# Kernel tuning notes

Hardware: AMD Instinct MI355X
Metric: run time of the kernel (lower is better)

The kernel has to match this reference:

```python
import jax, jax.numpy as jnp
import numpy as np


def mha_col0(x0, w_in, b_in, w_out, b_out):
    # x0: [N, D]. torch MHA (1 head, batch_first=False): seq dim = N, this is the
    # batch-0 slice (the only one consumed by tmp[:, 0]).
    qkv = x0 @ w_in.T + b_in                     # [N, 3D]
    q, k, v = jnp.split(qkv, 3, axis=-1)         # each [N, D]
    scale = 1.0 / np.sqrt(np.float32(q.shape[-1]))
    attn = jax.nn.softmax((q * scale) @ k.T, axis=-1)   # [N, N]
    return (attn @ v) @ w_out.T + b_out          # [N, D]


def sage(x_src, x_dst, ei, w_l, b_l, w_r):
    # PyG SAGEConv with aggr='sum': out = lin_l(sum_j x_src[src_j]) + lin_r(x_dst)
    msg = x_src[ei[0]]                                            # [E, D] gather
    agg = jax.ops.segment_sum(msg, ei[1], num_segments=x_dst.shape[0])  # [Nd, D] scatter
    return agg @ w_l.T + b_l + x_dst @ w_r.T


def setup_inputs() -> dict:
    key = jax.random.key(0)
    ks = jax.random.split(key, 24)
    N, C, D, E = 8192, 6, 128, 262144
    s = 0.05
    p = lambda k, shape: jax.random.normal(k, shape, dtype=jnp.float32) * s
    return {
        "x_A": jax.random.normal(ks[0], (N, C, D), dtype=jnp.float32),
        "x_B": jax.random.normal(ks[1], (N, C, D), dtype=jnp.float32),
        "ei_AB": jax.random.randint(ks[2], (2, E), 0, N),
        "ei_BA": jax.random.randint(ks[3], (2, E), 0, N),
        "ei_AA": jax.random.randint(ks[4], (2, E), 0, N),
        "inW_A": p(ks[5], (3 * D, D)), "inB_A": p(ks[6], (3 * D,)),
        "outW_A": p(ks[7], (D, D)), "outB_A": p(ks[8], (D,)),
        "inW_B": p(ks[9], (3 * D, D)), "inB_B": p(ks[10], (3 * D,)),
        "outW_B": p(ks[11], (D, D)), "outB_B": p(ks[12], (D,)),
        "wl_AB": p(ks[13], (D, D)), "bl_AB": p(ks[14], (D,)), "wr_AB": p(ks[15], (D, D)),
        "wl_BA": p(ks[16], (D, D)), "bl_BA": p(ks[17], (D,)), "wr_BA": p(ks[18], (D, D)),
        "wl_AA": p(ks[19], (D, D)), "bl_AA": p(ks[20], (D,)), "wr_AA": p(ks[21], (D, D)),
    }


def reference(x_A, x_B, ei_AB, ei_BA, ei_AA,
              inW_A, inB_A, outW_A, outB_A,
              inW_B, inB_B, outW_B, outB_B,
              wl_AB, bl_AB, wr_AB,
              wl_BA, bl_BA, wr_BA,
              wl_AA, bl_AA, wr_AA):
    # per-type attention, keeping only column 0 (tmp[:, 0])
    h_A = mha_col0(x_A[:, 0], inW_A, inB_A, outW_A, outB_A)   # [N, D]
    h_B = mha_col0(x_B[:, 0], inW_B, inB_B, outW_B, outB_B)   # [N, D]
    # HeteroConv(aggr='sum'): B gets A->B; A gets B->A + A->A
    out_B = sage(h_A, h_B, ei_AB, wl_AB, bl_AB, wr_AB)
    out_A = (sage(h_B, h_A, ei_BA, wl_BA, bl_BA, wr_BA)
             + sage(h_A, h_A, ei_AA, wl_AA, bl_AA, wr_AA))
    # re-attach remaining column tokens (x is 3D)
    new_A = jnp.concatenate((out_A[:, None, :], x_A[:, 1:]), axis=1)  # [N, C, D]
    new_B = jnp.concatenate((out_B[:, None, :], x_B[:, 1:]), axis=1)
    return new_A, new_B
```

## Files before the change

### kernel.cpp

```cpp
#include <hip/hip_runtime.h>
#include <hip/hip_bf16.h>

typedef unsigned short u16;
typedef unsigned int u32;
typedef __attribute__((ext_vector_type(8))) short bf16x8;
typedef __attribute__((ext_vector_type(4))) short bf16x4;
typedef __attribute__((ext_vector_type(4))) float f32x4;
typedef __attribute__((ext_vector_type(16))) float f32x16;

#define MFMA(a,b,c)   __builtin_amdgcn_mfma_f32_16x16x32_bf16((a),(b),(c),0,0,0)
#define MFMA32(a,b,c) __builtin_amdgcn_mfma_f32_32x32x16_bf16((a),(b),(c),0,0,0)

__device__ __forceinline__ float bf2f(u16 u){
  union { float f; u32 i; } c; c.i = ((u32)u) << 16; return c.f;
}
__device__ __forceinline__ u16 f2bf(float f){
  __hip_bfloat16 h = __float2bfloat16(f);
  u16 u; __builtin_memcpy(&u, &h, 2); return u;
}
__device__ __forceinline__ bf16x8 ld8f(const float* p){
  bf16x8 r;
  #pragma unroll
  for (int i = 0; i < 8; i++) r[i] = (short)f2bf(p[i]);
  return r;
}
__device__ __forceinline__ u32 cvtpk(float a, float b){
  u32 r; asm volatile("v_cvt_pk_bf16_f32 %0, %1, %2" : "=v"(r) : "v"(a), "v"(b)); return r;
}
__device__ __forceinline__ void pl32swap(u32 &a, u32 &b){
  asm volatile("v_permlane32_swap_b32 %0, %1" : "+v"(a), "+v"(b));
}

struct WPrepArgs { const float* src[10]; int off[10]; int total4; };
__global__ __launch_bounds__(256) void wprep_kernel(WPrepArgs a, u16* __restrict__ dst)
{
  int i = blockIdx.x * 256 + threadIdx.x;
  if (i >= a.total4) return;
  int e = i * 4;
  int j = 0;
  #pragma unroll
  for (int k = 1; k < 10; k++) if (e >= a.off[k]) j = k;
  const float* s = a.src[j] + (e - a.off[j]);
  f32x4 v = *(const f32x4*)s;
  bf16x4 o;
  #pragma unroll
  for (int r = 0; r < 4; r++) o[r] = (short)f2bf(v[r]);
  *(bf16x4*)(dst + e) = o;
}

template<int XBF>
__global__ __launch_bounds__(256) void linear_kernel(
    const void* __restrict__ xA_, const u16* __restrict__ wA, const float* __restrict__ bA, u16* __restrict__ yA,
    const void* __restrict__ xB_, const u16* __restrict__ wB, const float* __restrict__ bB, u16* __restrict__ yB,
    u16* __restrict__ vtA_, u16* __restrict__ vtB_,
    int xstride, int ystride, int M, int N)
{
  const void* x_ = blockIdx.y ? xB_ : xA_;
  const u16* w = blockIdx.y ? wB : wA;
  const float* b = blockIdx.y ? bB : bA;
  u16* y = blockIdx.y ? yB : yA;
  u16* vt = blockIdx.y ? vtB_ : vtA_;
  const int lane = threadIdx.x & 63, wid = threadIdx.x >> 6;
  const int g = lane >> 4, l15 = lane & 15;
  const int row0 = blockIdx.x * 64 + wid * 16;

  bf16x8 a[4];
  if (XBF) {
    const u16* xr = (const u16*)x_ + (size_t)(row0 + l15) * xstride;
    #pragma unroll
    for (int kk = 0; kk < 4; kk++) a[kk] = *(const bf16x8*)(xr + kk * 32 + g * 8);
  } else {
    const float* xr = (const float*)x_ + (size_t)(row0 + l15) * xstride;
    #pragma unroll
    for (int kk = 0; kk < 4; kk++) a[kk] = ld8f(xr + kk * 32 + g * 8);
  }

  const f32x4 fz = {0.f, 0.f, 0.f, 0.f};
  for (int j0 = 0; j0 < M; j0 += 16) {
    f32x4 acc = fz;
    const u16* wr_ = w + (size_t)(j0 + l15) * 128;
    #pragma unroll
    for (int kk = 0; kk < 4; kk++)
      acc = MFMA(a[kk], *(const bf16x8*)(wr_ + kk * 32 + g * 8), acc);
    float bv = b[j0 + l15];
    if (j0 < 256 || vt == nullptr) {
      #pragma unroll
      for (int r = 0; r < 4; r++)
        y[(size_t)(row0 + g * 4 + r) * ystride + j0 + l15] = f2bf(acc[r] + bv);
    } else {
      bf16x4 o4;
      #pragma unroll
      for (int r = 0; r < 4; r++) o4[r] = (short)f2bf(acc[r] + bv);
      *(bf16x4*)(vt + (size_t)(j0 - 256 + l15) * N + row0 + g * 4) = o4;
    }
  }
}

__global__ __launch_bounds__(256, 2) void flash_kernel(
    const u16* __restrict__ qkvA, const u16* __restrict__ vtA,
    const u16* __restrict__ qkvB, const u16* __restrict__ vtB,
    u16* __restrict__ part_acc, float* __restrict__ part_ml,
    int N, int segsz, int SEG)
{
  __shared__ __align__(16) u16 Kt[2][64 * 128];
  __shared__ __align__(16) u16 Vtt[2][128 * 64];
  const int ty = blockIdx.z;
  const u16* qkv = ty ? qkvB : qkvA;
  const u16* vt  = ty ? vtB  : vtA;
  const int tid = threadIdx.x;
  const int lane = tid & 63, wid = tid >> 6;
  const int l31 = lane & 31, h = lane >> 5, l7 = lane & 7;
  const int q = blockIdx.x * 128 + wid * 32 + l31;
  const int seg = blockIdx.y;
  const int kvbase = seg * segsz;
  const float C = 0.088388347648318447f * 1.4426950408889634f;
  const float THR = 8.0f / C;

  int rk[4], ck[4], cks[4], rv[4], cv[4], cvs[4];
  #pragma unroll
  for (int i = 0; i < 4; i++) {
    int ch = tid + i * 256;
    rk[i] = ch >> 4; ck[i] = (ch & 15) * 8; cks[i] = ck[i] ^ ((rk[i] & 7) << 3);
    rv[i] = ch >> 3; cv[i] = (ch & 7) * 8;  cvs[i] = cv[i] ^ ((rv[i] & 7) << 3);
  }

  bf16x8 aQ[8];
  const u16* qr = qkv + (size_t)q * 256;
  #pragma unroll
  for (int kk = 0; kk < 8; kk++) aQ[kk] = *(const bf16x8*)(qr + kk * 16 + h * 8);

  f32x16 accO[4];
  #pragma unroll
  for (int d = 0; d < 4; d++) accO[d] = (f32x16)0.f;
  float m_ = -INFINITY, l_ = 0.f;

  {
    #pragma unroll
    for (int i = 0; i < 4; i++) {
      bf16x8 kv8 = *(const bf16x8*)(qkv + 128 + (size_t)(kvbase + rk[i]) * 256 + ck[i]);
      bf16x8 vv8 = *(const bf16x8*)(vt + (size_t)rv[i] * N + kvbase + cv[i]);
      *(bf16x8*)&Kt[0][rk[i] * 128 + cks[i]] = kv8;
      *(bf16x8*)&Vtt[0][rv[i] * 64 + cvs[i]] = vv8;
    }
  }
  __syncthreads();

  int cur = 0;
  for (int kt = 0; kt < segsz; kt += 64) {
    const bool pfch = (kt + 64 < segsz);
    bf16x8 kreg[4], vreg[4];
    if (pfch) {
      const int kv0n = kvbase + kt + 64;
      #pragma unroll
      for (int i = 0; i < 4; i++) {
        kreg[i] = *(const bf16x8*)(qkv + 128 + (size_t)(kv0n + rk[i]) * 256 + ck[i]);
        vreg[i] = *(const bf16x8*)(vt + (size_t)rv[i] * N + kv0n + cv[i]);
      }
    }

    const u16* KtC = Kt[cur];
    const u16* VtC = Vtt[cur];

    f32x16 sc0 = (f32x16)0.f, sc1 = (f32x16)0.f;
    #pragma unroll
    for (int kk = 0; kk < 8; kk++) {
      const int co = ((kk * 2 + h) * 8) ^ (l7 << 3);
      bf16x8 aK0 = *(bf16x8*)&KtC[l31 * 128 + co];
      bf16x8 aK1 = *(bf16x8*)&KtC[(32 + l31) * 128 + co];
      sc0 = MFMA32(aK0, aQ[kk], sc0);
      sc1 = MFMA32(aK1, aQ[kk], sc1);
    }

    float pmax = sc0[0];
    #pragma unroll
    for (int i = 1; i < 16; i++) pmax = fmaxf(pmax, sc0[i]);
    #pragma unroll
    for (int i = 0; i < 16; i++) pmax = fmaxf(pmax, sc1[i]);
    pmax = fmaxf(pmax, __shfl_xor(pmax, 32));
    if (!__all(pmax - m_ <= THR)) {
      float nm = fmaxf(m_, pmax);
      float corr = __builtin_exp2f((m_ - nm) * C);
      m_ = nm; l_ *= corr;
      #pragma unroll
      for (int d = 0; d < 4; d++)
        #pragma unroll
        for (int i = 0; i < 16; i++) accO[d][i] *= corr;
    }
    float sum = 0.f;
    #pragma unroll
    for (int i = 0; i < 16; i++) {
      float e0 = __builtin_exp2f((sc0[i] - m_) * C);
      float e1 = __builtin_exp2f((sc1[i] - m_) * C);
      sc0[i] = e0; sc1[i] = e1; sum += e0 + e1;
    }
    sum += __shfl_xor(sum, 32);
    l_ += sum;

    #pragma unroll
    for (int t = 0; t < 4; t++) {
      const int jA = (t & 1) * 2, jB = jA + 1;
      u32 a0, b0, a1, b1;
      if (t < 2) {
        a0 = cvtpk(sc0[jA * 4 + 0], sc0[jA * 4 + 1]);
        b0 = cvtpk(sc0[jB * 4 + 0], sc0[jB * 4 + 1]);
        a1 = cvtpk(sc0[jA * 4 + 2], sc0[jA * 4 + 3]);
        b1 = cvtpk(sc0[jB * 4 + 2], sc0[jB * 4 + 3]);
      } else {
        a0 = cvtpk(sc1[jA * 4 + 0], sc1[jA * 4 + 1]);
        b0 = cvtpk(sc1[jB * 4 + 0], sc1[jB * 4 + 1]);
        a1 = cvtpk(sc1[jA * 4 + 2], sc1[jA * 4 + 3]);
        b1 = cvtpk(sc1[jB * 4 + 2], sc1[jB * 4 + 3]);
      }
      pl32swap(a0, b0); pl32swap(a1, b1);
      union { u32 w[4]; bf16x8 v; } pf;
      pf.w[0] = a0; pf.w[1] = a1; pf.w[2] = b0; pf.w[3] = b1;
      #pragma unroll
      for (int db = 0; db < 4; db++) {
        bf16x8 aV = *(bf16x8*)&VtC[(db * 32 + l31) * 64 + (((t * 2 + h) * 8) ^ (l7 << 3))];
        accO[db] = MFMA32(aV, pf.v, accO[db]);
      }
    }

    if (pfch) {
      const int nb = cur ^ 1;
      #pragma unroll
      for (int i = 0; i < 4; i++) {
        *(bf16x8*)&Kt[nb][rk[i] * 128 + cks[i]] = kreg[i];
        *(bf16x8*)&Vtt[nb][rv[i] * 64 + cvs[i]] = vreg[i];
      }
    }
    __syncthreads();
    cur ^= 1;
  }

  const size_t pbase = ((size_t)(ty * SEG + seg) * N + q) * 128;
  #pragma unroll
  for (int d = 0; d < 4; d++)
    #pragma unroll
    for (int j = 0; j < 4; j++) {
      bf16x4 o4;
      #pragma unroll
      for (int r = 0; r < 4; r++) o4[r] = (short)f2bf(accO[d][j * 4 + r]);
      *(bf16x4*)(part_acc + pbase + d * 32 + j * 8 + h * 4) = o4;
    }
  if (h == 0) {
    float2 ml; ml.x = m_; ml.y = l_;
    *(float2*)(part_ml + ((size_t)(ty * SEG + seg) * N + q) * 2) = ml;
  }
}

__global__ __launch_bounds__(256) void combine_hproj_kernel(
    const u16* __restrict__ part_acc, const float* __restrict__ part_ml,
    const u16* __restrict__ woutA, const float* __restrict__ boutA, u16* __restrict__ hA,
    const u16* __restrict__ woutB, const float* __restrict__ boutB, u16* __restrict__ hB,
    int N, int SEG)
{
  __shared__ __align__(16) u16 ot[64 * 136];
  const int t = blockIdx.y;
  const u16* w = t ? woutB : woutA;
  const float* bb = t ? boutB : boutA;
  u16* hOut = t ? hB : hA;
  const int tid = threadIdx.x;
  const int row = tid >> 2, qt = tid & 3;
  const int grow = blockIdx.x * 64 + row;
  const float C = 0.088388347648318447f * 1.4426950408889634f;

  float m = -INFINITY;
  for (int s = 0; s < SEG; s++)
    m = fmaxf(m, part_ml[((size_t)(t * SEG + s) * N + grow) * 2]);
  float l = 0.f;
  float acc[32];
  #pragma unroll
  for (int i = 0; i < 32; i++) acc[i] = 0.f;
  for (int s = 0; s < SEG; s++) {
    const float* ml = part_ml + ((size_t)(t * SEG + s) * N + grow) * 2;
    float w8 = __builtin_exp2f((ml[0] - m) * C);
    l += w8 * ml[1];
    const u16* pa = part_acc + ((size_t)(t * SEG + s) * N + grow) * 128 + qt * 32;
    #pragma unroll
    for (int j = 0; j < 4; j++) {
      bf16x8 vch = *(const bf16x8*)(pa + j * 8);
      #pragma unroll
      for (int i = 0; i < 8; i++) acc[j * 8 + i] += w8 * bf2f((u16)vch[i]);
    }
  }
  const float inv = 1.f / l;
  #pragma unroll
  for (int j = 0; j < 4; j++) {
    bf16x8 oc;
    #pragma unroll
    for (int i = 0; i < 8; i++) oc[i] = (short)f2bf(acc[j * 8 + i] * inv);
    *(bf16x8*)&ot[row * 136 + qt * 32 + j * 8] = oc;
  }
  __syncthreads();

  const int lane = tid & 63, wid = tid >> 6;
  const int g = lane >> 4, l15 = lane & 15;
  const int row0 = wid * 16;
  bf16x8 a[4];
  #pragma unroll
  for (int kk = 0; kk < 4; kk++) a[kk] = *(bf16x8*)&ot[(row0 + l15) * 136 + kk * 32 + g * 8];
  const f32x4 fz = {0.f, 0.f, 0.f, 0.f};
  for (int j0 = 0; j0 < 128; j0 += 16) {
    f32x4 acc2 = fz;
    const u16* wr_ = w + (size_t)(j0 + l15) * 128;
    #pragma unroll
    for (int kk = 0; kk < 4; kk++)
      acc2 = MFMA(a[kk], *(const bf16x8*)(wr_ + kk * 32 + g * 8), acc2);
    float bv = bb[j0 + l15];
    #pragma unroll
    for (int r = 0; r < 4; r++)
      hOut[(size_t)(blockIdx.x * 64 + row0 + g * 4 + r) * 128 + j0 + l15] = f2bf(acc2[r] + bv);
  }
}

__global__ __launch_bounds__(256) void hist_kernel(
    const int* __restrict__ e0, const int* __restrict__ e1, const int* __restrict__ e2,
    int* __restrict__ cnt, int Nn, int E)
{
  const int t = blockIdx.y;
  const int* ei = t == 0 ? e0 : (t == 1 ? e1 : e2);
  int e = blockIdx.x * 256 + threadIdx.x;
  if (e >= E) return;
  atomicAdd(&cnt[t * Nn + ei[E + e]], 1);
}

__global__ __launch_bounds__(1024) void scan_kernel(
    const int* __restrict__ cnt, int* __restrict__ off, int* __restrict__ work, int Nn)
{
  const int t = blockIdx.x;
  const int* c = cnt + t * Nn;
  int* o = off + t * (Nn + 1);
  int* w = work + t * Nn;
  __shared__ int part[1024];
  const int tid = threadIdx.x;
  const int base = tid * 8;
  int loc[8], s = 0;
  #pragma unroll
  for (int i = 0; i < 8; i++) { loc[i] = s; s += c[base + i]; }
  part[tid] = s;
  __syncthreads();
  #pragma unroll
  for (int st = 1; st < 1024; st <<= 1) {
    int v = (tid >= st) ? part[tid - st] : 0;
    __syncthreads();
    part[tid] += v;
    __syncthreads();
  }
  int pre = (tid == 0) ? 0 : part[tid - 1];
  #pragma unroll
  for (int i = 0; i < 8; i++) { int p = pre + loc[i]; o[base + i] = p; w[base + i] = p; }
  if (tid == 1023) o[Nn] = part[1023];
}

__global__ __launch_bounds__(256) void sortedges_kernel(
    const int* __restrict__ e0, const int* __restrict__ e1, const int* __restrict__ e2,
    int* __restrict__ work, int* __restrict__ ssrc, int Nn, int E)
{
  const int t = blockIdx.y;
  const int* ei = t == 0 ? e0 : (t == 1 ? e1 : e2);
  int e = blockIdx.x * 256 + threadIdx.x;
  if (e >= E) return;
  int s = ei[e], d = ei[E + e];
  int pos = atomicAdd(&work[t * Nn + d], 1);
  ssrc[(size_t)t * E + pos] = s;
}

__global__ __launch_bounds__(256) void aggregate_kernel(
    const u16* __restrict__ h0, const u16* __restrict__ h1, const u16* __restrict__ h2,
    const int* __restrict__ off, const int* __restrict__ ssrc,
    float* __restrict__ agg, int Nn, int E)
{
  const int t = blockIdx.y;
  const u16* h = t == 0 ? h0 : (t == 1 ? h1 : h2);
  const int* o = off + t * (Nn + 1);
  const int* ss = ssrc + (size_t)t * E;
  float* a = agg + (size_t)t * Nn * 128;
  const int wid = threadIdx.x >> 6, lane = threadIdx.x & 63;
  const int d = blockIdx.x * 4 + wid;
  const int s0 = o[d], s1 = o[d + 1];
  float a0 = 0.f, a1 = 0.f;
  int e = s0;
  for (; e + 3 < s1; e += 4) {
    int r0 = ss[e], r1 = ss[e + 1], r2 = ss[e + 2], r3 = ss[e + 3];
    u32 v0 = *(const u32*)(h + (size_t)r0 * 128 + lane * 2);
    u32 v1 = *(const u32*)(h + (size_t)r1 * 128 + lane * 2);
    u32 v2 = *(const u32*)(h + (size_t)r2 * 128 + lane * 2);
    u32 v3 = *(const u32*)(h + (size_t)r3 * 128 + lane * 2);
    a0 += bf2f((u16)(v0 & 0xffff)) + bf2f((u16)(v1 & 0xffff)) + bf2f((u16)(v2 & 0xffff)) + bf2f((u16)(v3 & 0xffff));
    a1 += bf2f((u16)(v0 >> 16)) + bf2f((u16)(v1 >> 16)) + bf2f((u16)(v2 >> 16)) + bf2f((u16)(v3 >> 16));
  }
  for (; e < s1; e++) {
    u32 v = *(const u32*)(h + (size_t)ss[e] * 128 + lane * 2);
    a0 += bf2f((u16)(v & 0xffff));
    a1 += bf2f((u16)(v >> 16));
  }
  a[(size_t)d * 128 + lane * 2] = a0;
  a[(size_t)d * 128 + lane * 2 + 1] = a1;
}

__global__ __launch_bounds__(256) void sage_out_kernel(
    const float* __restrict__ agg1, const u16* __restrict__ wl1, const float* __restrict__ bl1,
    const u16* __restrict__ h1, const u16* __restrict__ wr1,
    const float* __restrict__ agg2, const u16* __restrict__ wl2, const float* __restrict__ bl2,
    const u16* __restrict__ h2, const u16* __restrict__ wr2,
    float* __restrict__ out)
{
  const int lane = threadIdx.x & 63, wid = threadIdx.x >> 6;
  const int g = lane >> 4, l15 = lane & 15;
  const int row0 = blockIdx.x * 64 + wid * 16;
  const bool two = (agg2 != nullptr);

  bf16x8 a1[4], aH1[4], a2[4], aH2[4];
  const float* ar1 = agg1 + (size_t)(row0 + l15) * 128;
  const u16* hr1 = h1 + (size_t)(row0 + l15) * 128;
  #pragma unroll
  for (int kk = 0; kk < 4; kk++) {
    a1[kk] = ld8f(ar1 + kk * 32 + g * 8);
    aH1[kk] = *(const bf16x8*)(hr1 + kk * 32 + g * 8);
  }
  if (two) {
    const float* ar2 = agg2 + (size_t)(row0 + l15) * 128;
    const u16* hr2 = h2 + (size_t)(row0 + l15) * 128;
    #pragma unroll
    for (int kk = 0; kk < 4; kk++) {
      a2[kk] = ld8f(ar2 + kk * 32 + g * 8);
      aH2[kk] = *(const bf16x8*)(hr2 + kk * 32 + g * 8);
    }
  }

  const f32x4 fz = {0.f, 0.f, 0.f, 0.f};
  for (int j0 = 0; j0 < 128; j0 += 16) {
    f32x4 acc = fz;
    const u16* w1 = wl1 + (size_t)(j0 + l15) * 128;
    const u16* w2 = wr1 + (size_t)(j0 + l15) * 128;
    #pragma unroll
    for (int kk = 0; kk < 4; kk++) {
      acc = MFMA(a1[kk], *(const bf16x8*)(w1 + kk * 32 + g * 8), acc);
      acc = MFMA(aH1[kk], *(const bf16x8*)(w2 + kk * 32 + g * 8), acc);
    }
    float bias = bl1[j0 + l15];
    if (two) {
      const u16* w3 = wl2 + (size_t)(j0 + l15) * 128;
      const u16* w4 = wr2 + (size_t)(j0 + l15) * 128;
      #pragma unroll
      for (int kk = 0; kk < 4; kk++) {
        acc = MFMA(a2[kk], *(const bf16x8*)(w3 + kk * 32 + g * 8), acc);
        acc = MFMA(aH2[kk], *(const bf16x8*)(w4 + kk * 32 + g * 8), acc);
      }
      bias += bl2[j0 + l15];
    }
    #pragma unroll
    for (int r = 0; r < 4; r++)
      out[(size_t)(row0 + g * 4 + r) * 768 + j0 + l15] = acc[r] + bias;
  }
}

__global__ __launch_bounds__(256) void tail_kernel(
    const float* __restrict__ xA, float* __restrict__ oA,
    const float* __restrict__ xB, float* __restrict__ oB, int total)
{
  const float* x = blockIdx.y ? xB : xA;
  float* o = blockIdx.y ? oB : oA;
  int tid = blockIdx.x * 256 + threadIdx.x;
  if (tid >= total) return;
  int n = tid / 160, r = tid % 160;
  size_t off = (size_t)n * 768 + 128 + (size_t)r * 4;
  *(f32x4*)(o + off) = *(const f32x4*)(x + off);
}

extern "C" void kernel_launch(void* const* d_in, const int* in_sizes, int n_in,
                              void* d_out, int out_size, void* d_ws, size_t ws_size,
                              hipStream_t stream)
{
  const int D = 128, C = 6;
  const int N = in_sizes[0] / (C * D);
  const int E = in_sizes[2] / 2;

  const float* xA = (const float*)d_in[0];
  const float* xB = (const float*)d_in[1];
  const int* eiAB = (const int*)d_in[2];
  const int* eiBA = (const int*)d_in[3];
  const int* eiAA = (const int*)d_in[4];
  const float* inW_A  = (const float*)d_in[5];
  const float* inB_A  = (const float*)d_in[6];
  const float* outW_A = (const float*)d_in[7];
  const float* outB_A = (const float*)d_in[8];
  const float* inW_B  = (const float*)d_in[9];
  const float* inB_B  = (const float*)d_in[10];
  const float* outW_B = (const float*)d_in[11];
  const float* outB_B = (const float*)d_in[12];
  const float* wlAB = (const float*)d_in[13];
  const float* blAB = (const float*)d_in[14];
  const float* wrAB = (const float*)d_in[15];
  const float* wlBA = (const float*)d_in[16];
  const float* blBA = (const float*)d_in[17];
  const float* wrBA = (const float*)d_in[18];
  const float* wlAA = (const float*)d_in[19];
  const float* blAA = (const float*)d_in[20];
  const float* wrAA = (const float*)d_in[21];

  u16* qkvA = (u16*)d_ws;
  u16* qkvB = qkvA + (size_t)N * 256;
  u16* vtA  = qkvB + (size_t)N * 256;
  u16* vtB  = vtA + (size_t)D * N;
  u16* hA   = vtB + (size_t)D * N;
  u16* hB   = hA + (size_t)N * D;
  u16* wbf  = hB + (size_t)N * D;
  const int wsz[10] = {3*D*D, 3*D*D, D*D, D*D, D*D, D*D, D*D, D*D, D*D, D*D};
  const float* wsrc[10] = {inW_A, inW_B, outW_A, outW_B, wlAB, wrAB, wlBA, wrBA, wlAA, wrAA};
  WPrepArgs wp; int wtot = 0;
  for (int k = 0; k < 10; k++) { wp.src[k] = wsrc[k]; wp.off[k] = wtot; wtot += wsz[k]; }
  wp.total4 = wtot / 4;
  u16* w_inA  = wbf + wp.off[0];
  u16* w_inB  = wbf + wp.off[1];
  u16* w_outA = wbf + wp.off[2];
  u16* w_outB = wbf + wp.off[3];
  u16* w_wlAB = wbf + wp.off[4];
  u16* w_wrAB = wbf + wp.off[5];
  u16* w_wlBA = wbf + wp.off[6];
  u16* w_wrBA = wbf + wp.off[7];
  u16* w_wlAA = wbf + wp.off[8];
  u16* w_wrAA = wbf + wp.off[9];

  char* uni = (char*)(wbf + wtot);
  size_t base_b = (size_t)((char*)uni - (char*)d_ws);
  size_t aggsort_b = (size_t)3 * N * 128 * 4 + (size_t)(3 * N + 3 * (N + 1) + 3 * N) * 4 + (size_t)3 * E * 4;
  auto part_b = [&](int S){ return (size_t)2 * S * N * 128 * 2 + (size_t)2 * S * N * 2 * 4; };
  int SEG = 4;
  while (SEG > 1 && ws_size < base_b + (part_b(SEG) > aggsort_b ? part_b(SEG) : aggsort_b)) SEG >>= 1;
  const int segsz = N / SEG;
  u16* part_acc = (u16*)uni;
  float* part_ml = (float*)(part_acc + (size_t)2 * SEG * N * 128);
  float* aggAB = (float*)uni;
  float* aggBA = aggAB + (size_t)N * D;
  float* aggAA = aggBA + (size_t)N * D;
  int* cnt  = (int*)(aggAA + (size_t)N * D);
  int* off  = cnt + 3 * N;
  int* work = off + 3 * (N + 1);
  int* ssrc = work + 3 * N;

  float* outA = (float*)d_out;
  float* outB = outA + (size_t)N * C * D;

  dim3 blk(256);
  wprep_kernel<<<dim3((wp.total4 + 255) / 256), blk, 0, stream>>>(wp, wbf);
  linear_kernel<0><<<dim3(N / 64, 2), blk, 0, stream>>>(xA, w_inA, inB_A, qkvA,
                                                        xB, w_inB, inB_B, qkvB,
                                                        vtA, vtB, C * D, 256, 384, N);
  flash_kernel<<<dim3(N / 128, SEG, 2), blk, 0, stream>>>(qkvA, vtA, qkvB, vtB,
                                                          part_acc, part_ml, N, segsz, SEG);
  combine_hproj_kernel<<<dim3(N / 64, 2), blk, 0, stream>>>(part_acc, part_ml,
                                                            w_outA, outB_A, hA,
                                                            w_outB, outB_B, hB, N, SEG);
  (void)hipMemsetAsync(cnt, 0, (size_t)3 * N * sizeof(int), stream);
  hist_kernel<<<dim3((E + 255) / 256, 3), blk, 0, stream>>>(eiAB, eiBA, eiAA, cnt, N, E);
  scan_kernel<<<dim3(3), dim3(1024), 0, stream>>>(cnt, off, work, N);
  sortedges_kernel<<<dim3((E + 255) / 256, 3), blk, 0, stream>>>(eiAB, eiBA, eiAA, work, ssrc, N, E);
  aggregate_kernel<<<dim3(N / 4, 3), blk, 0, stream>>>(hA, hB, hA, off, ssrc, aggAB, N, E);
  sage_out_kernel<<<dim3(N / 64), blk, 0, stream>>>(aggAB, w_wlAB, blAB, hB, w_wrAB,
                                                    nullptr, nullptr, nullptr, nullptr, nullptr, outB);
  sage_out_kernel<<<dim3(N / 64), blk, 0, stream>>>(aggBA, w_wlBA, blBA, hA, w_wrBA,
                                                    aggAA, w_wlAA, blAA, hA, w_wrAA, outA);
  int total = N * 160;
  tail_kernel<<<dim3((total + 255) / 256, 2), blk, 0, stream>>>(xA, outA, xB, outB, total);
}
```

Baseline: 275.6 us.

## Fuse weight prep, histogram and tail copy into one prelude kernel; bf16 aggregates

Merges the weight bf16 conversion, edge-destination histogram and the passthrough copy of columns 1..C-1 into a single launch at the start. Edge sorting now runs before attention, and its buffers get their own workspace region so they no longer alias the flash partials. Aggregated neighbour sums are stored as bf16 instead of fp32, which halves their memory traffic and drops the convert step in sage_out. It also raises wave priority around the MFMA loops in the flash kernel. The risks are extra rounding of the aggregate sums and a larger fixed workspace footprint, which may reduce the SEG split.

```diff
diff --git a/kernel.cpp b/kernel.cpp
--- a/kernel.cpp
+++ b/kernel.cpp
@@ -32,20 +32,50 @@
 }
 
 struct WPrepArgs { const float* src[10]; int off[10]; int total4; };
-__global__ __launch_bounds__(256) void wprep_kernel(WPrepArgs a, u16* __restrict__ dst)
-{
-  int i = blockIdx.x * 256 + threadIdx.x;
-  if (i >= a.total4) return;
-  int e = i * 4;
-  int j = 0;
-  #pragma unroll
-  for (int k = 1; k < 10; k++) if (e >= a.off[k]) j = k;
-  const float* s = a.src[j] + (e - a.off[j]);
-  f32x4 v = *(const f32x4*)s;
-  bf16x4 o;
-  #pragma unroll
-  for (int r = 0; r < 4; r++) o[r] = (short)f2bf(v[r]);
-  *(bf16x4*)(dst + e) = o;
+__global__ __launch_bounds__(256) void prelude_kernel(
+    WPrepArgs a, u16* __restrict__ wdst,
+    const int* __restrict__ e0, const int* __restrict__ e1, const int* __restrict__ e2,
+    int* __restrict__ cnt,
+    const float* __restrict__ xA, float* __restrict__ outA,
+    const float* __restrict__ xB, float* __restrict__ outB,
+    int Nn, int E, int W, int HB, int TB)
+{
+  const int tid = threadIdx.x;
+  int b = blockIdx.x;
+  if (b < W) {
+    int i = b * 256 + tid;
+    if (i >= a.total4) return;
+    int e = i * 4;
+    int j = 0;
+    #pragma unroll
+    for (int k = 1; k < 10; k++) if (e >= a.off[k]) j = k;
+    f32x4 v = *(const f32x4*)(a.src[j] + (e - a.off[j]));
+    bf16x4 o;
+    #pragma unroll
+    for (int r = 0; r < 4; r++) o[r] = (short)f2bf(v[r]);
+    *(bf16x4*)(wdst + e) = o;
+    return;
+  }
+  b -= W;
+  if (b < 3 * HB) {
+    int t = b / HB;
+    int e = (b % HB) * 256 + tid;
+    if (e >= E) return;
+    const int* ei = t == 0 ? e0 : (t == 1 ? e1 : e2);
+    atomicAdd(&cnt[t * Nn + ei[E + e]], 1);
+    return;
+  }
+  b -= 3 * HB;
+  {
+    int t = b / TB;
+    int idx = (b % TB) * 256 + tid;
+    if (idx >= Nn * 160) return;
+    const float* x = t ? xB : xA;
+    float* o = t ? outB : outA;
+    int n = idx / 160, r = idx % 160;
+    size_t off = (size_t)n * 768 + 128 + (size_t)r * 4;
+    *(f32x4*)(o + off) = *(const f32x4*)(x + off);
+  }
 }
 
 template<int XBF>
@@ -162,6 +192,7 @@
     const u16* VtC = Vtt[cur];
 
     f32x16 sc0 = (f32x16)0.f, sc1 = (f32x16)0.f;
+    __builtin_amdgcn_s_setprio(1);
     #pragma unroll
     for (int kk = 0; kk < 8; kk++) {
       const int co = ((kk * 2 + h) * 8) ^ (l7 << 3);
@@ -170,6 +201,7 @@
       sc0 = MFMA32(aK0, aQ[kk], sc0);
       sc1 = MFMA32(aK1, aQ[kk], sc1);
     }
+    __builtin_amdgcn_s_setprio(0);
 
     float pmax = sc0[0];
     #pragma unroll
@@ -214,11 +246,13 @@
       pl32swap(a0, b0); pl32swap(a1, b1);
       union { u32 w[4]; bf16x8 v; } pf;
       pf.w[0] = a0; pf.w[1] = a1; pf.w[2] = b0; pf.w[3] = b1;
+      __builtin_amdgcn_s_setprio(1);
       #pragma unroll
       for (int db = 0; db < 4; db++) {
         bf16x8 aV = *(bf16x8*)&VtC[(db * 32 + l31) * 64 + (((t * 2 + h) * 8) ^ (l7 << 3))];
         accO[db] = MFMA32(aV, pf.v, accO[db]);
       }
+      __builtin_amdgcn_s_setprio(0);
     }
 
     if (pfch) {
@@ -314,17 +348,6 @@
   }
 }
 
-__global__ __launch_bounds__(256) void hist_kernel(
-    const int* __restrict__ e0, const int* __restrict__ e1, const int* __restrict__ e2,
-    int* __restrict__ cnt, int Nn, int E)
-{
-  const int t = blockIdx.y;
-  const int* ei = t == 0 ? e0 : (t == 1 ? e1 : e2);
-  int e = blockIdx.x * 256 + threadIdx.x;
-  if (e >= E) return;
-  atomicAdd(&cnt[t * Nn + ei[E + e]], 1);
-}
-
 __global__ __launch_bounds__(1024) void scan_kernel(
     const int* __restrict__ cnt, int* __restrict__ off, int* __restrict__ work, int Nn)
 {
@@ -369,13 +392,13 @@
 __global__ __launch_bounds__(256) void aggregate_kernel(
     const u16* __restrict__ h0, const u16* __restrict__ h1, const u16* __restrict__ h2,
     const int* __restrict__ off, const int* __restrict__ ssrc,
-    float* __restrict__ agg, int Nn, int E)
+    u16* __restrict__ agg, int Nn, int E)
 {
   const int t = blockIdx.y;
   const u16* h = t == 0 ? h0 : (t == 1 ? h1 : h2);
   const int* o = off + t * (Nn + 1);
   const int* ss = ssrc + (size_t)t * E;
-  float* a = agg + (size_t)t * Nn * 128;
+  u16* a = agg + (size_t)t * Nn * 128;
   const int wid = threadIdx.x >> 6, lane = threadIdx.x & 63;
   const int d = blockIdx.x * 4 + wid;
   const int s0 = o[d], s1 = o[d + 1];
@@ -395,14 +418,13 @@
     a0 += bf2f((u16)(v & 0xffff));
     a1 += bf2f((u16)(v >> 16));
   }
-  a[(size_t)d * 128 + lane * 2] = a0;
-  a[(size_t)d * 128 + lane * 2 + 1] = a1;
+  *(u32*)(a + (size_t)d * 128 + lane * 2) = cvtpk(a0, a1);
 }
 
 __global__ __launch_bounds__(256) void sage_out_kernel(
-    const float* __restrict__ agg1, const u16* __restrict__ wl1, const float* __restrict__ bl1,
+    const u16* __restrict__ agg1, const u16* __restrict__ wl1, const float* __restrict__ bl1,
     const u16* __restrict__ h1, const u16* __restrict__ wr1,
-    const float* __restrict__ agg2, const u16* __restrict__ wl2, const float* __restrict__ bl2,
+    const u16* __restrict__ agg2, const u16* __restrict__ wl2, const float* __restrict__ bl2,
     const u16* __restrict__ h2, const u16* __restrict__ wr2,
     float* __restrict__ out)
 {
@@ -412,19 +434,19 @@
   const bool two = (agg2 != nullptr);
 
   bf16x8 a1[4], aH1[4], a2[4], aH2[4];
-  const float* ar1 = agg1 + (size_t)(row0 + l15) * 128;
+  const u16* ar1 = agg1 + (size_t)(row0 + l15) * 128;
   const u16* hr1 = h1 + (size_t)(row0 + l15) * 128;
   #pragma unroll
   for (int kk = 0; kk < 4; kk++) {
-    a1[kk] = ld8f(ar1 + kk * 32 + g * 8);
+    a1[kk] = *(const bf16x8*)(ar1 + kk * 32 + g * 8);
     aH1[kk] = *(const bf16x8*)(hr1 + kk * 32 + g * 8);
   }
   if (two) {
-    const float* ar2 = agg2 + (size_t)(row0 + l15) * 128;
+    const u16* ar2 = agg2 + (size_t)(row0 + l15) * 128;
     const u16* hr2 = h2 + (size_t)(row0 + l15) * 128;
     #pragma unroll
     for (int kk = 0; kk < 4; kk++) {
-      a2[kk] = ld8f(ar2 + kk * 32 + g * 8);
+      a2[kk] = *(const bf16x8*)(ar2 + kk * 32 + g * 8);
       aH2[kk] = *(const bf16x8*)(hr2 + kk * 32 + g * 8);
     }
   }
@@ -454,19 +476,6 @@
     for (int r = 0; r < 4; r++)
       out[(size_t)(row0 + g * 4 + r) * 768 + j0 + l15] = acc[r] + bias;
   }
-}
-
-__global__ __launch_bounds__(256) void tail_kernel(
-    const float* __restrict__ xA, float* __restrict__ oA,
-    const float* __restrict__ xB, float* __restrict__ oB, int total)
-{
-  const float* x = blockIdx.y ? xB : xA;
-  float* o = blockIdx.y ? oB : oA;
-  int tid = blockIdx.x * 256 + threadIdx.x;
-  if (tid >= total) return;
-  int n = tid / 160, r = tid % 160;
-  size_t off = (size_t)n * 768 + 128 + (size_t)r * 4;
-  *(f32x4*)(o + off) = *(const f32x4*)(x + off);
 }
 
 extern "C" void kernel_launch(void* const* d_in, const int* in_sizes, int n_in,
@@ -523,28 +532,35 @@
   u16* w_wlAA = wbf + wp.off[8];
   u16* w_wrAA = wbf + wp.off[9];
 
-  char* uni = (char*)(wbf + wtot);
-  size_t base_b = (size_t)((char*)uni - (char*)d_ws);
-  size_t aggsort_b = (size_t)3 * N * 128 * 4 + (size_t)(3 * N + 3 * (N + 1) + 3 * N) * 4 + (size_t)3 * E * 4;
+  int* cnt  = (int*)(wbf + wtot);
+  int* off  = cnt + 3 * N;
+  int* work = off + 3 * (N + 1);
+  int* ssrc = work + 3 * N;
+  char* uni = (char*)(ssrc + 3 * E);
+  size_t base_b = (size_t)(uni - (char*)d_ws);
+  size_t agg_b = (size_t)3 * N * 128 * 2;
   auto part_b = [&](int S){ return (size_t)2 * S * N * 128 * 2 + (size_t)2 * S * N * 2 * 4; };
   int SEG = 4;
-  while (SEG > 1 && ws_size < base_b + (part_b(SEG) > aggsort_b ? part_b(SEG) : aggsort_b)) SEG >>= 1;
+  while (SEG > 1 && ws_size < base_b + (part_b(SEG) > agg_b ? part_b(SEG) : agg_b)) SEG >>= 1;
   const int segsz = N / SEG;
   u16* part_acc = (u16*)uni;
   float* part_ml = (float*)(part_acc + (size_t)2 * SEG * N * 128);
-  float* aggAB = (float*)uni;
-  float* aggBA = aggAB + (size_t)N * D;
-  float* aggAA = aggBA + (size_t)N * D;
-  int* cnt  = (int*)(aggAA + (size_t)N * D);
-  int* off  = cnt + 3 * N;
-  int* work = off + 3 * (N + 1);
-  int* ssrc = work + 3 * N;
+  u16* aggAB = (u16*)uni;
+  u16* aggBA = aggAB + (size_t)N * D;
+  u16* aggAA = aggBA + (size_t)N * D;
 
   float* outA = (float*)d_out;
   float* outB = outA + (size_t)N * C * D;
 
   dim3 blk(256);
-  wprep_kernel<<<dim3((wp.total4 + 255) / 256), blk, 0, stream>>>(wp, wbf);
+  const int W = (wp.total4 + 255) / 256;
+  const int HB = (E + 255) / 256;
+  const int TB = (N * 160 + 255) / 256;
+  (void)hipMemsetAsync(cnt, 0, (size_t)3 * N * sizeof(int), stream);
+  prelude_kernel<<<dim3(W + 3 * HB + 2 * TB), blk, 0, stream>>>(
+      wp, wbf, eiAB, eiBA, eiAA, cnt, xA, outA, xB, outB, N, E, W, HB, TB);
+  scan_kernel<<<dim3(3), dim3(1024), 0, stream>>>(cnt, off, work, N);
+  sortedges_kernel<<<dim3(HB, 3), blk, 0, stream>>>(eiAB, eiBA, eiAA, work, ssrc, N, E);
   linear_kernel<0><<<dim3(N / 64, 2), blk, 0, stream>>>(xA, w_inA, inB_A, qkvA,
                                                         xB, w_inB, inB_B, qkvB,
                                                         vtA, vtB, C * D, 256, 384, N);
@@ -553,15 +569,9 @@
   combine_hproj_kernel<<<dim3(N / 64, 2), blk, 0, stream>>>(part_acc, part_ml,
                                                             w_outA, outB_A, hA,
                                                             w_outB, outB_B, hB, N, SEG);
-  (void)hipMemsetAsync(cnt, 0, (size_t)3 * N * sizeof(int), stream);
-  hist_kernel<<<dim3((E + 255) / 256, 3), blk, 0, stream>>>(eiAB, eiBA, eiAA, cnt, N, E);
-  scan_kernel<<<dim3(3), dim3(1024), 0, stream>>>(cnt, off, work, N);
-  sortedges_kernel<<<dim3((E + 255) / 256, 3), blk, 0, stream>>>(eiAB, eiBA, eiAA, work, ssrc, N, E);
   aggregate_kernel<<<dim3(N / 4, 3), blk, 0, stream>>>(hA, hB, hA, off, ssrc, aggAB, N, E);
   sage_out_kernel<<<dim3(N / 64), blk, 0, stream>>>(aggAB, w_wlAB, blAB, hB, w_wrAB,
                                                     nullptr, nullptr, nullptr, nullptr, nullptr, outB);
   sage_out_kernel<<<dim3(N / 64), blk, 0, stream>>>(aggBA, w_wlBA, blBA, hA, w_wrBA,
                                                     aggAA, w_wlAA, blAA, hA, w_wrAA, outA);
-  int total = N * 160;
-  tail_kernel<<<dim3((total + 255) / 256, 2), blk, 0, stream>>>(xA, outA, xB, outB, total);
-}
+}
```

Measured after the change: 270.3 us. About the same (-1.9%).
